# Kernel optimization log

Hardware: AMD Instinct MI355X
Metric: run time of the kernel (lower is better)

## Reference

```python
import jax, jax.numpy as jnp
import numpy as np

B, C, H, W = 16, 256, 64, 64
DA = 64  # attention_size


def setup_inputs() -> dict:
    key = jax.random.key(0)
    ks = jax.random.split(key, 7)
    s_in = 1.0 / np.sqrt(C)
    return {
        "x": jax.random.normal(ks[0], (B, C, H, W), jnp.float32),
        "Wq": jax.random.normal(ks[1], (DA, C), jnp.float32) * s_in,
        "bq": jax.random.normal(ks[2], (DA,), jnp.float32) * 0.01,
        "Wk": jax.random.normal(ks[3], (DA, C), jnp.float32) * s_in,
        "bk": jax.random.normal(ks[4], (DA,), jnp.float32) * 0.01,
        "Wv": jax.random.normal(ks[5], (C, C), jnp.float32) * s_in,
        "bv": jax.random.normal(ks[6], (C,), jnp.float32) * 0.01,
    }


def reference(x, Wq, bq, Wk, bk, Wv, bv):
    b, c, h, w = x.shape
    n = h * w
    xf = x.reshape(b, c, n)                      # [B,C,N]
    q = jnp.einsum('ac,bcn->ban', Wq, xf) + bq[None, :, None]   # [B,DA,N]
    k = jnp.einsum('ac,bcn->ban', Wk, xf) + bk[None, :, None]   # [B,DA,N]
    v = jnp.einsum('dc,bcn->bdn', Wv, xf) + bv[None, :, None]   # [B,C,N]
    # scores[b,i,j] = q[:,i] . k[:,j], scaled by 1/sqrt(H*W) (as in source)
    scores = jnp.einsum('bai,baj->bij', q, k) / jnp.sqrt(jnp.float32(n))
    attn = jax.nn.softmax(scores, axis=-1)       # [B,N,N]
    out = jnp.einsum('bcj,bij->bci', v, attn)    # [B,C,N]
    return out.reshape(b, c, h, w) + x
```

## Files before the change

kernel.cpp:

```cpp
#include <hip/hip_runtime.h>
#include <hip/hip_bf16.h>
#include <stdint.h>


#define B_  16
#define C_  256
#define N_  4096
#define DA_ 64
#define MSHIFT 2.0f

typedef __attribute__((ext_vector_type(8))) short short8;
typedef __attribute__((ext_vector_type(4))) float f32x4;

__device__ int g_isf32;

__device__ __forceinline__ short f2bf(float f) {
    union { float f; uint32_t u; } v; v.f = f;
    uint32_t r = v.u + 0x7fffu + ((v.u >> 16) & 1u);
    return (short)(r >> 16);
}
__device__ __forceinline__ float bf2f(uint16_t s) {
    union { uint32_t u; float f; } v; v.u = ((uint32_t)s) << 16;
    return v.f;
}
__device__ __forceinline__ uint32_t pkbf(float a, float b) {
    union { __hip_bfloat162 h; uint32_t u; } c;
    c.h = __float22bfloat162_rn(make_float2(a, b));
    return c.u;
}

__global__ void detect_kernel(const void* __restrict__ x) {
    const uint16_t* p = (const uint16_t*)x;
    int i = threadIdx.x;
    uint16_t u = p[2 * i];
    int e = (u >> 7) & 0xFF;
    unsigned long long m = __ballot(e >= 112 && e <= 132);
    if (i == 0) g_isf32 = (__popcll(m) < 32) ? 1 : 0;
}

template<bool F32>
__device__ __forceinline__ void proj_body(
    const void* __restrict__ xv,
    const void* __restrict__ Wqv, const void* __restrict__ bqv,
    const void* __restrict__ Wkv, const void* __restrict__ bkv,
    const void* __restrict__ Wvv, const void* __restrict__ bvv,
    uint16_t* __restrict__ Q, uint16_t* __restrict__ K, uint16_t* __restrict__ Vt,
    float* bias_lds, uint16_t* buf)
{
    const int tid = threadIdx.x;
    const int b  = blockIdx.x >> 6;
    const int n0 = (blockIdx.x & 63) * 64;
    const int w = tid >> 6, lane = tid & 63, q = lane >> 4, ln = lane & 15;

    for (int idx = tid; idx < 384; idx += 256) {
        float bias;
        if (F32) {
            bias = (idx < 64)  ? ((const float*)bqv)[idx]
                 : (idx < 128) ? ((const float*)bkv)[idx - 64]
                               : ((const float*)bvv)[idx - 128];
        } else {
            bias = (idx < 64)  ? bf2f(((const uint16_t*)bqv)[idx])
                 : (idx < 128) ? bf2f(((const uint16_t*)bkv)[idx - 64])
                               : bf2f(((const uint16_t*)bvv)[idx - 128]);
        }
        bias_lds[idx] = bias;
    }

    {
        int cbase = tid >> 2, s0 = tid & 3;
        #pragma unroll
        for (int cc = 0; cc < 4; cc++) {
            int c = cc * 64 + cbase;
            if (F32) {
                const float* xr = (const float*)xv + ((size_t)b * C_ + c) * N_ + n0;
                #pragma unroll
                for (int k = 0; k < 4; k++) {
                    int nl = (s0 + 4 * k) * 4;
                    float4 v = *(const float4*)(xr + nl);
                    buf[(nl + 0) * 264 + c] = (uint16_t)f2bf(v.x);
                    buf[(nl + 1) * 264 + c] = (uint16_t)f2bf(v.y);
                    buf[(nl + 2) * 264 + c] = (uint16_t)f2bf(v.z);
                    buf[(nl + 3) * 264 + c] = (uint16_t)f2bf(v.w);
                }
            } else {
                const uint16_t* xr = (const uint16_t*)xv + ((size_t)b * C_ + c) * N_ + n0;
                #pragma unroll
                for (int k = 0; k < 2; k++) {
                    int nl = s0 * 16 + k * 8;
                    short8 v = *(const short8*)(xr + nl);
                    #pragma unroll
                    for (int e = 0; e < 8; e++)
                        buf[(nl + e) * 264 + c] = (uint16_t)v[e];
                }
            }
        }
    }
    __syncthreads();

    f32x4 acc[6][4];
    #pragma unroll
    for (int mt = 0; mt < 6; mt++)
        #pragma unroll
        for (int nt = 0; nt < 4; nt++) acc[mt][nt] = (f32x4)0.0f;

    for (int kc = 0; kc < 8; kc++) {
        short8 af[6];
        #pragma unroll
        for (int mt = 0; mt < 6; mt++) {
            int row = (w * 6 + mt) * 16 + ln;
            if (F32) {
                const float* src = (row < 64) ? (const float*)Wqv + (size_t)row * 256
                                 : (row < 128) ? (const float*)Wkv + (size_t)(row - 64) * 256
                                               : (const float*)Wvv + (size_t)(row - 128) * 256;
                float4 a0 = *(const float4*)(src + kc * 32 + q * 8);
                float4 a1 = *(const float4*)(src + kc * 32 + q * 8 + 4);
                union { short8 s; uint32_t u[4]; } c;
                c.u[0] = pkbf(a0.x, a0.y); c.u[1] = pkbf(a0.z, a0.w);
                c.u[2] = pkbf(a1.x, a1.y); c.u[3] = pkbf(a1.z, a1.w);
                af[mt] = c.s;
            } else {
                const uint16_t* src = (row < 64) ? (const uint16_t*)Wqv + (size_t)row * 256
                                    : (row < 128) ? (const uint16_t*)Wkv + (size_t)(row - 64) * 256
                                                  : (const uint16_t*)Wvv + (size_t)(row - 128) * 256;
                af[mt] = *(const short8*)(src + kc * 32 + q * 8);
            }
        }
        short8 bfr[4];
        #pragma unroll
        for (int nt = 0; nt < 4; nt++)
            bfr[nt] = *(const short8*)&buf[(nt * 16 + ln) * 264 + kc * 32 + q * 8];
        #pragma unroll
        for (int mt = 0; mt < 6; mt++)
            #pragma unroll
            for (int nt = 0; nt < 4; nt++)
                acc[mt][nt] = __builtin_amdgcn_mfma_f32_16x16x32_bf16(
                    af[mt], bfr[nt], acc[mt][nt], 0, 0, 0);
    }
    __syncthreads();

    #pragma unroll
    for (int mt = 0; mt < 6; mt++) {
        int rowb = (w * 6 + mt) * 16 + q * 4;
        #pragma unroll
        for (int r = 0; r < 4; r++) {
            float bias = bias_lds[rowb + r];
            #pragma unroll
            for (int nt = 0; nt < 4; nt++)
                buf[(rowb + r) * 72 + nt * 16 + ln] =
                    (uint16_t)f2bf(acc[mt][nt][r] + bias);
        }
    }
    __syncthreads();

    {
        int a = tid & 63, nb = tid >> 6;
        uint16_t* Qb = Q + ((size_t)b * N_ + n0) * 64;
        uint16_t* Kb = K + ((size_t)b * N_ + n0) * 64;
        #pragma unroll 4
        for (int j = 0; j < 16; j++) {
            int n = nb + 4 * j;
            Qb[(size_t)n * 64 + a] = buf[a * 72 + n];
            Kb[(size_t)n * 64 + a] = buf[(64 + a) * 72 + n];
        }
    }
    {
        int ch = tid & 7;
        #pragma unroll
        for (int p = 0; p < 8; p++) {
            int c = p * 32 + (tid >> 3);
            short8 v = *(const short8*)&buf[(128 + c) * 72 + ch * 8];
            *(short8*)(Vt + ((size_t)b * C_ + c) * N_ + n0 + ch * 8) = v;
        }
    }
}

__global__ __launch_bounds__(256, 2) void proj_kernel(
    const void* xv, const void* Wqv, const void* bqv, const void* Wkv,
    const void* bkv, const void* Wvv, const void* bvv,
    uint16_t* Q, uint16_t* K, uint16_t* Vt)
{
    __shared__ float    bias_lds[384];
    __shared__ uint16_t buf[384 * 72];
    if (g_isf32) proj_body<true >(xv, Wqv, bqv, Wkv, bkv, Wvv, bvv, Q, K, Vt, bias_lds, buf);
    else         proj_body<false>(xv, Wqv, bqv, Wkv, bkv, Wvv, bvv, Q, K, Vt, bias_lds, buf);
}

template<bool F32>
__device__ __forceinline__ void flash_body(
    const uint16_t* __restrict__ Q, const uint16_t* __restrict__ K,
    const uint16_t* __restrict__ Vt, const void* __restrict__ xv,
    void* __restrict__ outv,
    uint16_t* Klds2, uint16_t* Plds2, float* l_lds)
{
    const int tid = threadIdx.x;
    const int d  = blockIdx.x;
    const int xc = d & 7, rest = d >> 3;
    const int b  = xc + ((rest >= 64) ? 8 : 0);
    const int i0 = (rest & 63) * 64;
    const int w = tid >> 6, lane = tid & 63, q = lane >> 4, ln = lane & 15;

    const float c1 = 1.4426950408889634f / 64.0f;

    short8 qf[2];
    {
        const uint16_t* qrow = Q + ((size_t)b * N_ + (i0 + w * 16 + ln)) * 64;
        qf[0] = *(const short8*)(qrow + q * 8);
        qf[1] = *(const short8*)(qrow + 32 + q * 8);
    }

    const uint16_t* Kb = K + (size_t)b * N_ * 64;
    const uint16_t* vr0 = Vt + ((size_t)b * C_ + (w * 64 +  0 + ln)) * N_ + q * 8;
    const uint16_t* vr1 = Vt + ((size_t)b * C_ + (w * 64 + 16 + ln)) * N_ + q * 8;
    const uint16_t* vr2 = Vt + ((size_t)b * C_ + (w * 64 + 32 + ln)) * N_ + q * 8;
    const uint16_t* vr3 = Vt + ((size_t)b * C_ + (w * 64 + 48 + ln)) * N_ + q * 8;

    const int krow = tid >> 2, kch = (tid & 3) * 16;

    float l_run = 0.0f;
    f32x4 O[4][4];
    #pragma unroll
    for (int rg = 0; rg < 4; rg++)
        #pragma unroll
        for (int ct = 0; ct < 4; ct++) O[rg][ct] = (f32x4)0.0f;

    {
        short8 k0 = *(const short8*)(Kb + (size_t)krow * 64 + kch);
        short8 k1 = *(const short8*)(Kb + (size_t)krow * 64 + kch + 8);
        *(short8*)&Klds2[krow * 72 + kch]     = k0;
        *(short8*)&Klds2[krow * 72 + kch + 8] = k1;
    }
    __syncthreads();

    for (int it = 0; it < 64; it++) {
        const int j0 = it * 64;
        const int cur = it & 1;
        const uint16_t* Kc = Klds2 + cur * (64 * 72);
        uint16_t*       Kn = Klds2 + (cur ^ 1) * (64 * 72);
        uint16_t*       Pl = Plds2 + cur * (64 * 72);

        short8 v00 = *(const short8*)(vr0 + j0);
        short8 v01 = *(const short8*)(vr1 + j0);
        short8 v02 = *(const short8*)(vr2 + j0);
        short8 v03 = *(const short8*)(vr3 + j0);
        short8 v10 = *(const short8*)(vr0 + j0 + 32);
        short8 v11 = *(const short8*)(vr1 + j0 + 32);
        short8 v12 = *(const short8*)(vr2 + j0 + 32);
        short8 v13 = *(const short8*)(vr3 + j0 + 32);

        short8 kreg0, kreg1;
        if (it < 63) {
            kreg0 = *(const short8*)(Kb + (size_t)(j0 + 64 + krow) * 64 + kch);
            kreg1 = *(const short8*)(Kb + (size_t)(j0 + 64 + krow) * 64 + kch + 8);
        }

        f32x4 s[4];
        #pragma unroll
        for (int jt = 0; jt < 4; jt++) s[jt] = (f32x4)0.0f;
        #pragma unroll
        for (int jt = 0; jt < 4; jt++) {
            short8 kf0 = *(const short8*)&Kc[(jt * 16 + ln) * 72 + q * 8];
            s[jt] = __builtin_amdgcn_mfma_f32_16x16x32_bf16(kf0, qf[0], s[jt], 0, 0, 0);
            short8 kf1 = *(const short8*)&Kc[(jt * 16 + ln) * 72 + 32 + q * 8];
            s[jt] = __builtin_amdgcn_mfma_f32_16x16x32_bf16(kf1, qf[1], s[jt], 0, 0, 0);
        }

        uint16_t* prow = &Pl[(w * 16 + ln) * 72 + q * 4];
        #pragma unroll
        for (int jt = 0; jt < 4; jt++) {
            float p0 = exp2f(s[jt][0] * c1 - MSHIFT);
            float p1 = exp2f(s[jt][1] * c1 - MSHIFT);
            float p2 = exp2f(s[jt][2] * c1 - MSHIFT);
            float p3 = exp2f(s[jt][3] * c1 - MSHIFT);
            l_run += (p0 + p1) + (p2 + p3);
            uint2 pk; pk.x = pkbf(p0, p1); pk.y = pkbf(p2, p3);
            *(uint2*)&prow[jt * 16] = pk;
        }

        asm volatile("s_waitcnt lgkmcnt(0)\n\ts_barrier" ::: "memory");

        {
            short8 af[4];
            #pragma unroll
            for (int rg = 0; rg < 4; rg++)
                af[rg] = *(const short8*)&Pl[(rg * 16 + ln) * 72 + q * 8];
            #pragma unroll
            for (int rg = 0; rg < 4; rg++) {
                O[rg][0] = __builtin_amdgcn_mfma_f32_16x16x32_bf16(af[rg], v00, O[rg][0], 0, 0, 0);
                O[rg][1] = __builtin_amdgcn_mfma_f32_16x16x32_bf16(af[rg], v01, O[rg][1], 0, 0, 0);
                O[rg][2] = __builtin_amdgcn_mfma_f32_16x16x32_bf16(af[rg], v02, O[rg][2], 0, 0, 0);
                O[rg][3] = __builtin_amdgcn_mfma_f32_16x16x32_bf16(af[rg], v03, O[rg][3], 0, 0, 0);
            }
            #pragma unroll
            for (int rg = 0; rg < 4; rg++)
                af[rg] = *(const short8*)&Pl[(rg * 16 + ln) * 72 + 32 + q * 8];
            #pragma unroll
            for (int rg = 0; rg < 4; rg++) {
                O[rg][0] = __builtin_amdgcn_mfma_f32_16x16x32_bf16(af[rg], v10, O[rg][0], 0, 0, 0);
                O[rg][1] = __builtin_amdgcn_mfma_f32_16x16x32_bf16(af[rg], v11, O[rg][1], 0, 0, 0);
                O[rg][2] = __builtin_amdgcn_mfma_f32_16x16x32_bf16(af[rg], v12, O[rg][2], 0, 0, 0);
                O[rg][3] = __builtin_amdgcn_mfma_f32_16x16x32_bf16(af[rg], v13, O[rg][3], 0, 0, 0);
            }
        }

        if (it < 63) {
            asm volatile("s_waitcnt vmcnt(0)" ::: "memory");
            *(short8*)&Kn[krow * 72 + kch]     = kreg0;
            *(short8*)&Kn[krow * 72 + kch + 8] = kreg1;
        }
        asm volatile("s_waitcnt lgkmcnt(0)\n\ts_barrier" ::: "memory");
    }

    l_run += __shfl_xor(l_run, 16);
    l_run += __shfl_xor(l_run, 32);
    if (lane < 16) l_lds[w * 16 + lane] = l_run;
    __syncthreads();

    #pragma unroll
    for (int rg = 0; rg < 4; rg++) {
        f32x4 lv = *(const f32x4*)&l_lds[rg * 16 + q * 4];
        f32x4 li; li[0] = 1.0f/lv[0]; li[1] = 1.0f/lv[1]; li[2] = 1.0f/lv[2]; li[3] = 1.0f/lv[3];
        #pragma unroll
        for (int ct = 0; ct < 4; ct++) {
            int c = w * 64 + ct * 16 + ln;
            size_t off = (size_t)c * N_ + i0 + rg * 16 + q * 4;
            if (F32) {
                const float* xb = (const float*)xv + (size_t)b * C_ * N_;
                float* ob = (float*)outv + (size_t)b * C_ * N_;
                float4 xv4 = *(const float4*)(xb + off);
                float4 res;
                res.x = O[rg][ct][0] * li[0] + xv4.x;
                res.y = O[rg][ct][1] * li[1] + xv4.y;
                res.z = O[rg][ct][2] * li[2] + xv4.z;
                res.w = O[rg][ct][3] * li[3] + xv4.w;
                *(float4*)(ob + off) = res;
            } else {
                const uint16_t* xb = (const uint16_t*)xv + (size_t)b * C_ * N_;
                uint16_t* ob = (uint16_t*)outv + (size_t)b * C_ * N_;
                uint2 xp = *(const uint2*)(xb + off);
                uint2 res;
                res.x = pkbf(O[rg][ct][0] * li[0] + bf2f((uint16_t)(xp.x & 0xFFFF)),
                             O[rg][ct][1] * li[1] + bf2f((uint16_t)(xp.x >> 16)));
                res.y = pkbf(O[rg][ct][2] * li[2] + bf2f((uint16_t)(xp.y & 0xFFFF)),
                             O[rg][ct][3] * li[3] + bf2f((uint16_t)(xp.y >> 16)));
                *(uint2*)(ob + off) = res;
            }
        }
    }
}

__global__ __launch_bounds__(256, 3) void flash_kernel(
    const uint16_t* Q, const uint16_t* K, const uint16_t* Vt,
    const void* xv, void* outv)
{
    __shared__ uint16_t Klds2[2 * 64 * 72];
    __shared__ uint16_t Plds2[2 * 64 * 72];
    __shared__ __align__(16) float l_lds[64];
    if (g_isf32) flash_body<true >(Q, K, Vt, xv, outv, Klds2, Plds2, l_lds);
    else         flash_body<false>(Q, K, Vt, xv, outv, Klds2, Plds2, l_lds);
}

extern "C" void kernel_launch(void* const* d_in, const int* in_sizes, int n_in,
                              void* d_out, int out_size, void* d_ws, size_t ws_size,
                              hipStream_t stream) {
    const void* x  = d_in[0];
    const void* Wq = d_in[1];
    const void* bq = d_in[2];
    const void* Wk = d_in[3];
    const void* bk = d_in[4];
    const void* Wv = d_in[5];
    const void* bv = d_in[6];

    uint16_t* Qw = (uint16_t*)d_ws;
    uint16_t* Kw = Qw + (size_t)B_ * N_ * DA_;
    uint16_t* Vw = Kw + (size_t)B_ * N_ * DA_;

    detect_kernel<<<dim3(1), dim3(64), 0, stream>>>(x);
    proj_kernel<<<dim3(B_ * 64), dim3(256), 0, stream>>>(x, Wq, bq, Wk, bk, Wv, bv, Qw, Kw, Vw);
    flash_kernel<<<dim3(B_ * 64), dim3(256), 0, stream>>>(Qw, Kw, Vw, x, d_out);
}
```

Before: 442.7 us.

## Load K fragments directly from global memory instead of staging through LDS

```diff
diff --git a/kernel.cpp b/kernel.cpp
--- a/kernel.cpp
+++ b/kernel.cpp
@@ -190,7 +190,7 @@
     const uint16_t* __restrict__ Q, const uint16_t* __restrict__ K,
     const uint16_t* __restrict__ Vt, const void* __restrict__ xv,
     void* __restrict__ outv,
-    uint16_t* Klds2, uint16_t* Plds2, float* l_lds)
+    uint16_t* Plds2, float* l_lds)
 {
     const int tid = threadIdx.x;
     const int d  = blockIdx.x;
@@ -208,14 +208,12 @@
         qf[1] = *(const short8*)(qrow + 32 + q * 8);
     }
 
-    const uint16_t* Kb = K + (size_t)b * N_ * 64;
+    const uint16_t* kfb = K + (size_t)b * N_ * 64 + (size_t)ln * 64 + q * 8;
     const uint16_t* vr0 = Vt + ((size_t)b * C_ + (w * 64 +  0 + ln)) * N_ + q * 8;
     const uint16_t* vr1 = Vt + ((size_t)b * C_ + (w * 64 + 16 + ln)) * N_ + q * 8;
     const uint16_t* vr2 = Vt + ((size_t)b * C_ + (w * 64 + 32 + ln)) * N_ + q * 8;
     const uint16_t* vr3 = Vt + ((size_t)b * C_ + (w * 64 + 48 + ln)) * N_ + q * 8;
 
-    const int krow = tid >> 2, kch = (tid & 3) * 16;
-
     float l_run = 0.0f;
     f32x4 O[4][4];
     #pragma unroll
@@ -223,20 +221,18 @@
         #pragma unroll
         for (int ct = 0; ct < 4; ct++) O[rg][ct] = (f32x4)0.0f;
 
-    {
-        short8 k0 = *(const short8*)(Kb + (size_t)krow * 64 + kch);
-        short8 k1 = *(const short8*)(Kb + (size_t)krow * 64 + kch + 8);
-        *(short8*)&Klds2[krow * 72 + kch]     = k0;
-        *(short8*)&Klds2[krow * 72 + kch + 8] = k1;
-    }
-    __syncthreads();
-
     for (int it = 0; it < 64; it++) {
         const int j0 = it * 64;
         const int cur = it & 1;
-        const uint16_t* Kc = Klds2 + cur * (64 * 72);
-        uint16_t*       Kn = Klds2 + (cur ^ 1) * (64 * 72);
-        uint16_t*       Pl = Plds2 + cur * (64 * 72);
+        uint16_t* Pl = Plds2 + cur * (64 * 72);
+
+        const uint16_t* kt = kfb + (size_t)j0 * 64;
+        short8 kf[8];
+        #pragma unroll
+        for (int jt = 0; jt < 4; jt++) {
+            kf[2 * jt]     = *(const short8*)(kt + jt * 1024);
+            kf[2 * jt + 1] = *(const short8*)(kt + jt * 1024 + 32);
+        }
 
         short8 v00 = *(const short8*)(vr0 + j0);
         short8 v01 = *(const short8*)(vr1 + j0);
@@ -247,21 +243,13 @@
         short8 v12 = *(const short8*)(vr2 + j0 + 32);
         short8 v13 = *(const short8*)(vr3 + j0 + 32);
 
-        short8 kreg0, kreg1;
-        if (it < 63) {
-            kreg0 = *(const short8*)(Kb + (size_t)(j0 + 64 + krow) * 64 + kch);
-            kreg1 = *(const short8*)(Kb + (size_t)(j0 + 64 + krow) * 64 + kch + 8);
-        }
-
         f32x4 s[4];
         #pragma unroll
         for (int jt = 0; jt < 4; jt++) s[jt] = (f32x4)0.0f;
         #pragma unroll
         for (int jt = 0; jt < 4; jt++) {
-            short8 kf0 = *(const short8*)&Kc[(jt * 16 + ln) * 72 + q * 8];
-            s[jt] = __builtin_amdgcn_mfma_f32_16x16x32_bf16(kf0, qf[0], s[jt], 0, 0, 0);
-            short8 kf1 = *(const short8*)&Kc[(jt * 16 + ln) * 72 + 32 + q * 8];
-            s[jt] = __builtin_amdgcn_mfma_f32_16x16x32_bf16(kf1, qf[1], s[jt], 0, 0, 0);
+            s[jt] = __builtin_amdgcn_mfma_f32_16x16x32_bf16(kf[2 * jt],     qf[0], s[jt], 0, 0, 0);
+            s[jt] = __builtin_amdgcn_mfma_f32_16x16x32_bf16(kf[2 * jt + 1], qf[1], s[jt], 0, 0, 0);
         }
 
         uint16_t* prow = &Pl[(w * 16 + ln) * 72 + q * 4];
@@ -301,13 +289,6 @@
                 O[rg][3] = __builtin_amdgcn_mfma_f32_16x16x32_bf16(af[rg], v13, O[rg][3], 0, 0, 0);
             }
         }
-
-        if (it < 63) {
-            asm volatile("s_waitcnt vmcnt(0)" ::: "memory");
-            *(short8*)&Kn[krow * 72 + kch]     = kreg0;
-            *(short8*)&Kn[krow * 72 + kch + 8] = kreg1;
-        }
-        asm volatile("s_waitcnt lgkmcnt(0)\n\ts_barrier" ::: "memory");
     }
 
     l_run += __shfl_xor(l_run, 16);
@@ -352,11 +333,10 @@
     const uint16_t* Q, const uint16_t* K, const uint16_t* Vt,
     const void* xv, void* outv)
 {
-    __shared__ uint16_t Klds2[2 * 64 * 72];
     __shared__ uint16_t Plds2[2 * 64 * 72];
     __shared__ __align__(16) float l_lds[64];
-    if (g_isf32) flash_body<true >(Q, K, Vt, xv, outv, Klds2, Plds2, l_lds);
-    else         flash_body<false>(Q, K, Vt, xv, outv, Klds2, Plds2, l_lds);
+    if (g_isf32) flash_body<true >(Q, K, Vt, xv, outv, Plds2, l_lds);
+    else         flash_body<false>(Q, K, Vt, xv, outv, Plds2, l_lds);
 }
 
 extern "C" void kernel_launch(void* const* d_in, const int* in_sizes, int n_in,
```

Result: slower. 637.0 us (+43.9%).

## Store K and P tiles in MFMA fragment order and drop one barrier per iteration

Applied to the files above, without the earlier changes.

```diff
diff --git a/kernel.cpp b/kernel.cpp
--- a/kernel.cpp
+++ b/kernel.cpp
@@ -214,7 +214,11 @@
     const uint16_t* vr2 = Vt + ((size_t)b * C_ + (w * 64 + 32 + ln)) * N_ + q * 8;
     const uint16_t* vr3 = Vt + ((size_t)b * C_ + (w * 64 + 48 + ln)) * N_ + q * 8;
 
-    const int krow = tid >> 2, kch = (tid & 3) * 16;
+    const int krow = tid >> 2, kc4 = tid & 3;
+    const size_t kgoff = (size_t)krow * 64 + (size_t)(kc4 * 8);
+    const int kg0 = ((krow >> 4) * 128 + kc4 * 16 + (krow & 15)) * 8;
+
+    const int pbase = (w * 128 + (q >> 1) * 16 + ln) * 8 + (q & 1) * 4;
 
     float l_run = 0.0f;
     f32x4 O[4][4];
@@ -224,19 +228,25 @@
         for (int ct = 0; ct < 4; ct++) O[rg][ct] = (f32x4)0.0f;
 
     {
-        short8 k0 = *(const short8*)(Kb + (size_t)krow * 64 + kch);
-        short8 k1 = *(const short8*)(Kb + (size_t)krow * 64 + kch + 8);
-        *(short8*)&Klds2[krow * 72 + kch]     = k0;
-        *(short8*)&Klds2[krow * 72 + kch + 8] = k1;
+        short8 k0 = *(const short8*)(Kb + kgoff);
+        short8 k1 = *(const short8*)(Kb + kgoff + 32);
+        *(short8*)&Klds2[kg0]       = k0;
+        *(short8*)&Klds2[kg0 + 512] = k1;
     }
     __syncthreads();
 
     for (int it = 0; it < 64; it++) {
         const int j0 = it * 64;
         const int cur = it & 1;
-        const uint16_t* Kc = Klds2 + cur * (64 * 72);
-        uint16_t*       Kn = Klds2 + (cur ^ 1) * (64 * 72);
-        uint16_t*       Pl = Plds2 + cur * (64 * 72);
+        const uint16_t* Kc = Klds2 + cur * 4096;
+        uint16_t*       Kn = Klds2 + (cur ^ 1) * 4096;
+        uint16_t*       Pl = Plds2 + cur * 4096;
+
+        short8 kreg0, kreg1;
+        if (it < 63) {
+            kreg0 = *(const short8*)(Kb + (size_t)(j0 + 64) * 64 + kgoff);
+            kreg1 = *(const short8*)(Kb + (size_t)(j0 + 64) * 64 + kgoff + 32);
+        }
 
         short8 v00 = *(const short8*)(vr0 + j0);
         short8 v01 = *(const short8*)(vr1 + j0);
@@ -247,24 +257,17 @@
         short8 v12 = *(const short8*)(vr2 + j0 + 32);
         short8 v13 = *(const short8*)(vr3 + j0 + 32);
 
-        short8 kreg0, kreg1;
-        if (it < 63) {
-            kreg0 = *(const short8*)(Kb + (size_t)(j0 + 64 + krow) * 64 + kch);
-            kreg1 = *(const short8*)(Kb + (size_t)(j0 + 64 + krow) * 64 + kch + 8);
-        }
-
         f32x4 s[4];
         #pragma unroll
         for (int jt = 0; jt < 4; jt++) s[jt] = (f32x4)0.0f;
         #pragma unroll
         for (int jt = 0; jt < 4; jt++) {
-            short8 kf0 = *(const short8*)&Kc[(jt * 16 + ln) * 72 + q * 8];
+            short8 kf0 = *(const short8*)&Kc[lane * 8 + jt * 1024];
             s[jt] = __builtin_amdgcn_mfma_f32_16x16x32_bf16(kf0, qf[0], s[jt], 0, 0, 0);
-            short8 kf1 = *(const short8*)&Kc[(jt * 16 + ln) * 72 + 32 + q * 8];
+            short8 kf1 = *(const short8*)&Kc[lane * 8 + jt * 1024 + 512];
             s[jt] = __builtin_amdgcn_mfma_f32_16x16x32_bf16(kf1, qf[1], s[jt], 0, 0, 0);
         }
 
-        uint16_t* prow = &Pl[(w * 16 + ln) * 72 + q * 4];
         #pragma unroll
         for (int jt = 0; jt < 4; jt++) {
             float p0 = exp2f(s[jt][0] * c1 - MSHIFT);
@@ -273,7 +276,13 @@
             float p3 = exp2f(s[jt][3] * c1 - MSHIFT);
             l_run += (p0 + p1) + (p2 + p3);
             uint2 pk; pk.x = pkbf(p0, p1); pk.y = pkbf(p2, p3);
-            *(uint2*)&prow[jt * 16] = pk;
+            *(uint2*)&Pl[pbase + jt * 256] = pk;
+        }
+
+        if (it < 63) {
+            asm volatile("s_waitcnt vmcnt(0)" ::: "memory");
+            *(short8*)&Kn[kg0]       = kreg0;
+            *(short8*)&Kn[kg0 + 512] = kreg1;
         }
 
         asm volatile("s_waitcnt lgkmcnt(0)\n\ts_barrier" ::: "memory");
@@ -282,7 +291,7 @@
             short8 af[4];
             #pragma unroll
             for (int rg = 0; rg < 4; rg++)
-                af[rg] = *(const short8*)&Pl[(rg * 16 + ln) * 72 + q * 8];
+                af[rg] = *(const short8*)&Pl[lane * 8 + rg * 1024];
             #pragma unroll
             for (int rg = 0; rg < 4; rg++) {
                 O[rg][0] = __builtin_amdgcn_mfma_f32_16x16x32_bf16(af[rg], v00, O[rg][0], 0, 0, 0);
@@ -292,7 +301,7 @@
             }
             #pragma unroll
             for (int rg = 0; rg < 4; rg++)
-                af[rg] = *(const short8*)&Pl[(rg * 16 + ln) * 72 + 32 + q * 8];
+                af[rg] = *(const short8*)&Pl[lane * 8 + rg * 1024 + 512];
             #pragma unroll
             for (int rg = 0; rg < 4; rg++) {
                 O[rg][0] = __builtin_amdgcn_mfma_f32_16x16x32_bf16(af[rg], v10, O[rg][0], 0, 0, 0);
@@ -301,13 +310,6 @@
                 O[rg][3] = __builtin_amdgcn_mfma_f32_16x16x32_bf16(af[rg], v13, O[rg][3], 0, 0, 0);
             }
         }
-
-        if (it < 63) {
-            asm volatile("s_waitcnt vmcnt(0)" ::: "memory");
-            *(short8*)&Kn[krow * 72 + kch]     = kreg0;
-            *(short8*)&Kn[krow * 72 + kch + 8] = kreg1;
-        }
-        asm volatile("s_waitcnt lgkmcnt(0)\n\ts_barrier" ::: "memory");
     }
 
     l_run += __shfl_xor(l_run, 16);
@@ -352,8 +354,8 @@
     const uint16_t* Q, const uint16_t* K, const uint16_t* Vt,
     const void* xv, void* outv)
 {
-    __shared__ uint16_t Klds2[2 * 64 * 72];
-    __shared__ uint16_t Plds2[2 * 64 * 72];
+    __shared__ uint16_t Klds2[2 * 4096];
+    __shared__ uint16_t Plds2[2 * 4096];
     __shared__ __align__(16) float l_lds[64];
     if (g_isf32) flash_body<true >(Q, K, Vt, xv, outv, Klds2, Plds2, l_lds);
     else         flash_body<false>(Q, K, Vt, xv, outv, Klds2, Plds2, l_lds);
```

After: 435.2 us. About the same (-1.7%).
